# Kernel optimization log

Hardware: AMD Instinct MI355X
Metric: run time of the kernel (lower is better)

The kernel has to match this reference:

```python
import jax, jax.numpy as jnp
import numpy as np

N = 50000      # total nodes across all graphs
E = 1600000    # edges
G = 500        # graphs in batch
F = 128        # input node features
K = 5          # Chebyshev order


def setup_inputs() -> dict:
    key = jax.random.key(0)
    ks = jax.random.split(key, 12)
    x = jax.random.normal(ks[0], (N, F), dtype=jnp.float32)
    edge_index = jax.random.randint(ks[1], (2, E), 0, N)
    edge_attr = jax.random.uniform(ks[2], (E,), dtype=jnp.float32)
    batch = jnp.sort(jax.random.randint(ks[3], (N,), 0, G))
    s = 0.05
    W1 = jax.random.normal(ks[4], (K, F, 64), dtype=jnp.float32) * s
    b1 = jnp.zeros((64,), jnp.float32)
    W2 = jax.random.normal(ks[5], (K, 64, 64), dtype=jnp.float32) * s
    b2 = jnp.zeros((64,), jnp.float32)
    W3 = jax.random.normal(ks[6], (K, 64, 128), dtype=jnp.float32) * s
    b3 = jnp.zeros((128,), jnp.float32)
    Wl = jax.random.normal(ks[7], (128, 2), dtype=jnp.float32) * s
    bl = jnp.zeros((2,), jnp.float32)
    return {"x": x, "edge_index": edge_index, "edge_attr": edge_attr,
            "batch": batch, "W1": W1, "b1": b1, "W2": W2, "b2": b2,
            "W3": W3, "b3": b3, "Wl": Wl, "bl": bl}


def _cheb_conv(x, src, dst, w, Wk, b):
    """PyG ChebConv with lambda_max=2, sym norm: Lhat = -D^-1/2 A D^-1/2
    (the +I diag of L cancels the -I of the rescale, so only off-diag edges).
    Chebyshev recursion: Tx0=x, Tx1=Lhat x, Tx_k = 2 Lhat Tx_{k-1} - Tx_{k-2}."""
    n = x.shape[0]

    def prop(h):  # sparse matvec: out[i] = sum_{e: dst=i} w_e * h[src_e]
        return jax.ops.segment_sum(w[:, None] * h[src], dst, num_segments=n)

    Tx0 = x
    out = Tx0 @ Wk[0]
    Tx1 = prop(Tx0)
    out = out + Tx1 @ Wk[1]
    for k in range(2, Wk.shape[0]):
        Tx2 = 2.0 * prop(Tx1) - Tx0
        out = out + Tx2 @ Wk[k]
        Tx0, Tx1 = Tx1, Tx2
    return out + b


def reference(x, edge_index, edge_attr, batch, W1, b1, W2, b2, W3, b3, Wl, bl):
    src, dst = edge_index[0], edge_index[1]
    # sym-normalized scaled Laplacian edge weights (off-diagonal part)
    deg = jax.ops.segment_sum(edge_attr, src, num_segments=N)
    deg_safe = jnp.where(deg > 0, deg, 1.0)
    dinv = jnp.where(deg > 0, deg_safe ** -0.5, 0.0)
    w = -dinv[src] * edge_attr * dinv[dst]

    h = jax.nn.relu(_cheb_conv(x, src, dst, w, W1, b1))
    # dropout is identity at inference (training=False)
    h = jax.nn.relu(_cheb_conv(h, src, dst, w, W2, b2))
    h = jax.nn.relu(_cheb_conv(h, src, dst, w, W3, b3))

    # global_mean_pool over batch vector
    cnt = jax.ops.segment_sum(jnp.ones((N,), h.dtype), batch, num_segments=G)
    pooled = jax.ops.segment_sum(h, batch, num_segments=G) / jnp.maximum(cnt, 1.0)[:, None]

    logits = pooled @ Wl + bl
    return jax.nn.log_softmax(logits, axis=1)
```

## Files before the change

### kernel.cpp

```cpp
#include <hip/hip_runtime.h>
#include <hip/hip_bf16.h>

#define NN 50000
#define EE 1600000
#define GG 500

typedef __bf16 bf16x8 __attribute__((ext_vector_type(8)));
typedef float  f32x4  __attribute__((ext_vector_type(4)));

__device__ __forceinline__ float b2f(ushort u) {
  return __uint_as_float(((unsigned)u) << 16);
}
__device__ __forceinline__ ushort f2b(float f) {
  unsigned u = __float_as_uint(f);
  unsigned r = (u + 0x7fff + ((u >> 16) & 1)) >> 16;
  return (ushort)r;
}
__device__ __forceinline__ float lo16(uint v) { return __uint_as_float(v << 16); }
__device__ __forceinline__ float hi16(uint v) { return __uint_as_float(v & 0xffff0000u); }


__global__ void deg_hist_kernel(const int* __restrict__ src, const int* __restrict__ dst,
                                const float* __restrict__ ea, float* __restrict__ deg,
                                int* __restrict__ cnt, int* __restrict__ rank, int e) {
  int i = blockIdx.x * blockDim.x + threadIdx.x;
  if (i < e) {
    atomicAdd(&deg[src[i]], ea[i]);
    rank[i] = atomicAdd(&cnt[dst[i]], 1);
  }
}

__global__ void dinv_kernel(float* __restrict__ deg, int n) {
  int i = blockIdx.x * blockDim.x + threadIdx.x;
  if (i < n) { float d = deg[i]; deg[i] = (d > 0.f) ? (1.0f / sqrtf(d)) : 0.f; }
}

__global__ void scan1(const int* __restrict__ cnt, int* __restrict__ partial,
                      int* __restrict__ bsum, int n) {
  __shared__ int s[256];
  int t = threadIdx.x, i = blockIdx.x * 256 + t;
  int v = (i < n) ? ((cnt[i] + 7) & ~7) : 0;
  s[t] = v; __syncthreads();
  for (int off = 1; off < 256; off <<= 1) {
    int xv = (t >= off) ? s[t - off] : 0;
    __syncthreads(); s[t] += xv; __syncthreads();
  }
  if (i < n) partial[i] = s[t];
  if (t == 255) bsum[blockIdx.x] = s[255];
}

__global__ void scan2(int* __restrict__ bsum, int nb) {
  __shared__ int s[256];
  int t = threadIdx.x;
  int v = (t < nb) ? bsum[t] : 0;
  s[t] = v; __syncthreads();
  for (int off = 1; off < 256; off <<= 1) {
    int xv = (t >= off) ? s[t - off] : 0;
    __syncthreads(); s[t] += xv; __syncthreads();
  }
  if (t < nb) bsum[t] = s[t];
}

__global__ void scan3(const int* __restrict__ partial, const int* __restrict__ bsum,
                      int* __restrict__ rowptr, int n) {
  int i = blockIdx.x * 256 + threadIdx.x;
  if (i < n) {
    int off = (blockIdx.x > 0) ? bsum[blockIdx.x - 1] : 0;
    rowptr[i + 1] = partial[i] + off;
    if (i == 0) rowptr[0] = 0;
  }
}

__global__ void scatter_kernel(const int* __restrict__ src, const int* __restrict__ dst,
                               const float* __restrict__ ea, const float* __restrict__ dinv,
                               const int* __restrict__ rowptr, const int* __restrict__ rank,
                               uint2* __restrict__ edges, int e) {
  int i = blockIdx.x * blockDim.x + threadIdx.x;
  if (i < e) {
    int s = src[i], d = dst[i];
    float w = -dinv[s] * ea[i] * dinv[d];
    edges[rowptr[d] + rank[i]] = make_uint2((unsigned)s, __float_as_uint(w));
  }
}

__global__ void pad_kernel(const int* __restrict__ rowptr, const int* __restrict__ cnt,
                           uint2* __restrict__ edges, int n) {
  int i = blockIdx.x * 256 + threadIdx.x;
  if (i < n) {
    int c = cnt[i], p = (c + 7) & ~7, base = rowptr[i];
    for (int q = c; q < p; ++q) edges[base + q] = make_uint2(0u, 0u);
  }
}


__global__ void cvt_x(const float* __restrict__ x, ushort* __restrict__ xb, int n4) {
  int i = blockIdx.x * 256 + threadIdx.x;
  if (i < n4) {
    float4 v = ((const float4*)x)[i];
    ushort4 o;
    o.x = f2b(v.x); o.y = f2b(v.y); o.z = f2b(v.z); o.w = f2b(v.w);
    ((ushort4*)xb)[i] = o;
  }
}

__global__ void cvt_w(const float* __restrict__ W1, const float* __restrict__ W2,
                      const float* __restrict__ W3, ushort* __restrict__ Wt1,
                      ushort* __restrict__ Wt2, ushort* __restrict__ Wt3) {
  int i = blockIdx.x * 256 + threadIdx.x;
  if (i < 320 * 128) {
    int j = i / 128, k = i % 128;
    Wt1[i] = f2b(W1[((size_t)(j >> 6) * 128 + k) * 64 + (j & 63)]);
  } else if (i < 320 * 128 + 320 * 64) {
    int t = i - 320 * 128; int j = t / 64, k = t % 64;
    Wt2[t] = f2b(W2[((size_t)(j >> 6) * 64 + k) * 64 + (j & 63)]);
  } else if (i < 320 * 128 + 320 * 64 + 128 * 320) {
    int t = i - 320 * 128 - 320 * 64; int j = t / 320, k = t % 320;
    Wt3[t] = f2b(W3[(size_t)k * 128 + j]);
  }
}


template<int NADD, bool RELUB>
__global__ __launch_bounds__(256) void prop_kernel(
    const int* __restrict__ rowptr, const uint2* __restrict__ edges,
    const ushort* __restrict__ g, int sg,
    const ushort* __restrict__ a1, int sa1, float c1,
    const ushort* __restrict__ a2, int sa2, float c2,
    const float* __restrict__ bias,
    ushort* __restrict__ out, int so, int n, float alpha)
{
  int wv = blockIdx.x * 4 + (threadIdx.x >> 6);
  wv = __builtin_amdgcn_readfirstlane(wv);
  const int lane = threadIdx.x & 63;
  const int grp = lane >> 3;
  const int sub = lane & 7;
  if (wv >= n) return;
  const int e0 = __builtin_amdgcn_readfirstlane(rowptr[wv]);
  const int e1 = __builtin_amdgcn_readfirstlane(rowptr[wv + 1]);

  float ra[8] = {}, rb[8] = {};
  int j = e0;
  for (; j + 16 <= e1; j += 16) {
    uint2 pa = edges[j + grp];
    uint2 pb = edges[j + 8 + grp];
    uint4 va = *(const uint4*)&g[(size_t)pa.x * sg + sub * 8];
    uint4 vb = *(const uint4*)&g[(size_t)pb.x * sg + sub * 8];
    float wa = __uint_as_float(pa.y);
    float wb = __uint_as_float(pb.y);
    ra[0] += wa * lo16(va.x); ra[1] += wa * hi16(va.x);
    ra[2] += wa * lo16(va.y); ra[3] += wa * hi16(va.y);
    ra[4] += wa * lo16(va.z); ra[5] += wa * hi16(va.z);
    ra[6] += wa * lo16(va.w); ra[7] += wa * hi16(va.w);
    rb[0] += wb * lo16(vb.x); rb[1] += wb * hi16(vb.x);
    rb[2] += wb * lo16(vb.y); rb[3] += wb * hi16(vb.y);
    rb[4] += wb * lo16(vb.z); rb[5] += wb * hi16(vb.z);
    rb[6] += wb * lo16(vb.w); rb[7] += wb * hi16(vb.w);
  }
  if (j < e1) {
    uint2 p = edges[j + grp];
    uint4 v = *(const uint4*)&g[(size_t)p.x * sg + sub * 8];
    float w = __uint_as_float(p.y);
    ra[0] += w * lo16(v.x); ra[1] += w * hi16(v.x);
    ra[2] += w * lo16(v.y); ra[3] += w * hi16(v.y);
    ra[4] += w * lo16(v.z); ra[5] += w * hi16(v.z);
    ra[6] += w * lo16(v.w); ra[7] += w * hi16(v.w);
  }
  float r[8];
  #pragma unroll
  for (int e = 0; e < 8; ++e) {
    float t = ra[e] + rb[e];
    t += __shfl_xor(t, 8, 64);
    t += __shfl_xor(t, 16, 64);
    t += __shfl_xor(t, 32, 64);
    r[e] = alpha * t;
  }
  if constexpr (NADD >= 1) {
    uint4 u = *(const uint4*)&a1[(size_t)wv * sa1 + sub * 8];
    r[0] += c1 * lo16(u.x); r[1] += c1 * hi16(u.x);
    r[2] += c1 * lo16(u.y); r[3] += c1 * hi16(u.y);
    r[4] += c1 * lo16(u.z); r[5] += c1 * hi16(u.z);
    r[6] += c1 * lo16(u.w); r[7] += c1 * hi16(u.w);
  }
  if constexpr (NADD >= 2) {
    uint4 u = *(const uint4*)&a2[(size_t)wv * sa2 + sub * 8];
    r[0] += c2 * lo16(u.x); r[1] += c2 * hi16(u.x);
    r[2] += c2 * lo16(u.y); r[3] += c2 * hi16(u.y);
    r[4] += c2 * lo16(u.z); r[5] += c2 * hi16(u.z);
    r[6] += c2 * lo16(u.w); r[7] += c2 * hi16(u.w);
  }
  if constexpr (RELUB) {
    float4 b0 = *(const float4*)&bias[sub * 8];
    float4 b1 = *(const float4*)&bias[sub * 8 + 4];
    r[0] = fmaxf(r[0] + b0.x, 0.f); r[1] = fmaxf(r[1] + b0.y, 0.f);
    r[2] = fmaxf(r[2] + b0.z, 0.f); r[3] = fmaxf(r[3] + b0.w, 0.f);
    r[4] = fmaxf(r[4] + b1.x, 0.f); r[5] = fmaxf(r[5] + b1.y, 0.f);
    r[6] = fmaxf(r[6] + b1.z, 0.f); r[7] = fmaxf(r[7] + b1.w, 0.f);
  }
  if (grp == 0) {
    uint4 o;
    o.x = (uint)f2b(r[0]) | ((uint)f2b(r[1]) << 16);
    o.y = (uint)f2b(r[2]) | ((uint)f2b(r[3]) << 16);
    o.z = (uint)f2b(r[4]) | ((uint)f2b(r[5]) << 16);
    o.w = (uint)f2b(r[6]) | ((uint)f2b(r[7]) << 16);
    *(uint4*)&out[(size_t)wv * so + sub * 8] = o;
  }
}


template<int Ci, int Co, bool BR>
__global__ __launch_bounds__(256) void gemm_mfma(const ushort* __restrict__ A,
    const ushort* __restrict__ Wt, const float* __restrict__ bias,
    ushort* __restrict__ C, int n)
{
  const int lane = threadIdx.x & 63;
  const int wid  = threadIdx.x >> 6;
  const int rb = blockIdx.x * 256;
  const int cb = blockIdx.y * 64;
  const int lr = lane & 15;
  const int lk = (lane >> 4) << 3;
  f32x4 acc[4][4] = {};

  for (int kc = 0; kc < Ci; kc += 64) {
    bf16x8 bfrag[2][4];
    #pragma unroll
    for (int ks = 0; ks < 2; ++ks)
      #pragma unroll
      for (int nt = 0; nt < 4; ++nt)
        bfrag[ks][nt] = *(const bf16x8*)&Wt[(size_t)(cb + nt * 16 + lr) * Ci + kc + ks * 32 + lk];
    #pragma unroll
    for (int s = 0; s < 4; ++s) {
      const int row = rb + (wid * 4 + s) * 16 + lr;
      const ushort* ap = &A[(size_t)row * Ci + kc + lk];
      #pragma unroll
      for (int ks = 0; ks < 2; ++ks) {
        bf16x8 af = {};
        if (row < n) af = *(const bf16x8*)(ap + ks * 32);
        #pragma unroll
        for (int nt = 0; nt < 4; ++nt)
          acc[s][nt] = __builtin_amdgcn_mfma_f32_16x16x32_bf16(af, bfrag[ks][nt], acc[s][nt], 0, 0, 0);
      }
    }
  }

  #pragma unroll
  for (int s = 0; s < 4; ++s) {
    #pragma unroll
    for (int nt = 0; nt < 4; ++nt) {
      const int col = cb + nt * 16 + lr;
      #pragma unroll
      for (int r = 0; r < 4; ++r) {
        const int row = rb + (wid * 4 + s) * 16 + ((lane >> 4) << 2) + r;
        if (row < n) {
          float v = acc[s][nt][r];
          if constexpr (BR) v = fmaxf(v + bias[col], 0.f);
          C[(size_t)row * Co + col] = f2b(v);
        }
      }
    }
  }
}


__global__ __launch_bounds__(128) void pool_kernel(const ushort* __restrict__ h,
    const int* __restrict__ batch, float* __restrict__ pooled,
    float* __restrict__ gcnt, int n) {
  const int f = threadIdx.x;
  const int i0 = blockIdx.x * 64;
  const int iend = min(i0 + 64, n);
  int cur = batch[i0];
  float acc = 0.f;
  int run = 0;
  for (int i = i0; i < iend; ++i) {
    int b = batch[i];
    float v = b2f(h[(size_t)i * 128 + f]);
    if (b != cur) {
      atomicAdd(&pooled[cur * 128 + f], acc);
      if (f == 0) atomicAdd(&gcnt[cur], (float)run);
      acc = 0.f; run = 0; cur = b;
    }
    acc += v; run++;
  }
  atomicAdd(&pooled[cur * 128 + f], acc);
  if (f == 0) atomicAdd(&gcnt[cur], (float)run);
}

__global__ __launch_bounds__(128) void head_kernel(const float* __restrict__ pooled,
    const float* __restrict__ gcnt, const float* __restrict__ Wl,
    const float* __restrict__ bl, float* __restrict__ outp)
{
  int g = blockIdx.x, t = threadIdx.x;
  float denom = fmaxf(gcnt[g], 1.f);
  float p = pooled[g * 128 + t] / denom;
  __shared__ float s0[128], s1[128];
  s0[t] = p * Wl[t * 2 + 0];
  s1[t] = p * Wl[t * 2 + 1];
  __syncthreads();
  for (int off = 64; off > 0; off >>= 1) {
    if (t < off) { s0[t] += s0[t + off]; s1[t] += s1[t + off]; }
    __syncthreads();
  }
  if (t == 0) {
    float a = s0[0] + bl[0], b = s1[0] + bl[1];
    float m = fmaxf(a, b);
    float z = logf(expf(a - m) + expf(b - m)) + m;
    outp[g * 2 + 0] = a - z;
    outp[g * 2 + 1] = b - z;
  }
}


extern "C" void kernel_launch(void* const* d_in, const int* in_sizes, int n_in,
                              void* d_out, int out_size, void* d_ws, size_t ws_size,
                              hipStream_t stream) {
  const float* x   = (const float*)d_in[0];
  const int*   ei  = (const int*)d_in[1];
  const float* ea  = (const float*)d_in[2];
  const int* batch = (const int*)d_in[3];
  const float* W1  = (const float*)d_in[4];
  const float* lb1 = (const float*)d_in[5];
  const float* W2  = (const float*)d_in[6];
  const float* lb2 = (const float*)d_in[7];
  const float* W3  = (const float*)d_in[8];
  const float* lb3 = (const float*)d_in[9];
  const float* Wl  = (const float*)d_in[10];
  const float* bl  = (const float*)d_in[11];
  const int* srcv = ei;
  const int* dstv = ei + EE;

  char* w = (char*)d_ws;
  auto alloc = [&](size_t bytes) -> char* {
    char* p = w; w += (bytes + 255) & ~(size_t)255; return p;
  };
  float* deg    = (float*)alloc((size_t)NN * 4);
  int*   rowptr = (int*)alloc((size_t)(NN + 1) * 4);
  int*   cnt    = (int*)alloc((size_t)NN * 4);
  int*   bsum   = (int*)alloc(256 * 4);
  int*   rank   = (int*)alloc((size_t)EE * 4);
  uint2* edges  = (uint2*)alloc((size_t)(EE + 8 * NN) * 8);
  ushort* xb    = (ushort*)alloc((size_t)NN * 128 * 2);
  ushort* Acat  = (ushort*)alloc((size_t)NN * 320 * 2);
  ushort* Bcat  = (ushort*)alloc((size_t)NN * 320 * 2);
  ushort* h1    = (ushort*)alloc((size_t)NN * 64 * 2);
  ushort* Wt1   = (ushort*)alloc((size_t)320 * 128 * 2);
  ushort* Wt2   = (ushort*)alloc((size_t)320 * 64 * 2);
  ushort* Wt3   = (ushort*)alloc((size_t)128 * 320 * 2);
  float* pooled = (float*)alloc((size_t)(GG * 128 + GG) * 4);
  float* gcnt   = pooled + GG * 128;
  int*   partial = (int*)Acat;
  ushort* h3 = Bcat;

  hipMemsetAsync(deg, 0, (size_t)NN * 4, stream);
  hipMemsetAsync(cnt, 0, (size_t)NN * 4, stream);
  hipMemsetAsync(pooled, 0, (size_t)(GG * 128 + GG) * 4, stream);

  deg_hist_kernel<<<(EE + 255) / 256, 256, 0, stream>>>(srcv, dstv, ea, deg, cnt, rank, EE);
  dinv_kernel<<<(NN + 255) / 256, 256, 0, stream>>>(deg, NN);
  const int nb = (NN + 255) / 256;
  scan1<<<nb, 256, 0, stream>>>(cnt, partial, bsum, NN);
  scan2<<<1, 256, 0, stream>>>(bsum, nb);
  scan3<<<nb, 256, 0, stream>>>(partial, bsum, rowptr, NN);
  scatter_kernel<<<(EE + 255) / 256, 256, 0, stream>>>(srcv, dstv, ea, deg, rowptr, rank,
                                                       edges, EE);
  pad_kernel<<<nb, 256, 0, stream>>>(rowptr, cnt, edges, NN);

  cvt_x<<<(NN * 128 / 4 + 255) / 256, 256, 0, stream>>>(x, xb, NN * 128 / 4);
  cvt_w<<<(320 * 128 + 320 * 64 + 128 * 320 + 255) / 256, 256, 0, stream>>>(
      W1, W2, W3, Wt1, Wt2, Wt3);

  const int PG = (NN + 3) / 4;
  const int GX = (NN + 255) / 256;

  ushort* A0 = Acat + 0 * 64;  ushort* A1 = Acat + 1 * 64;  ushort* A2 = Acat + 2 * 64;
  ushort* A3 = Acat + 3 * 64;  ushort* A4 = Acat + 4 * 64;
  ushort* B0 = Bcat + 0 * 64;  ushort* B1 = Bcat + 1 * 64;  ushort* B2 = Bcat + 2 * 64;
  ushort* B3 = Bcat + 3 * 64;  ushort* B4 = Bcat + 4 * 64;
  const int S = 320;

  gemm_mfma<128, 320, false><<<dim3(GX, 5), 256, 0, stream>>>(xb, Wt1, nullptr, Acat, NN);
  prop_kernel<1, false><<<PG, 256, 0, stream>>>(rowptr, edges, A4, S, A3, S, 1.f,
      nullptr, 0, 0.f, nullptr, A3, S, NN, 2.f);
  prop_kernel<2, false><<<PG, 256, 0, stream>>>(rowptr, edges, A3, S, A2, S, 1.f,
      A4, S, -1.f, nullptr, A2, S, NN, 2.f);
  prop_kernel<2, false><<<PG, 256, 0, stream>>>(rowptr, edges, A2, S, A1, S, 1.f,
      A3, S, -1.f, nullptr, A1, S, NN, 2.f);
  prop_kernel<2, true><<<PG, 256, 0, stream>>>(rowptr, edges, A1, S, A0, S, 1.f,
      A2, S, -1.f, lb1, h1, 64, NN, 1.f);

  gemm_mfma<64, 320, false><<<dim3(GX, 5), 256, 0, stream>>>(h1, Wt2, nullptr, Bcat, NN);
  prop_kernel<1, false><<<PG, 256, 0, stream>>>(rowptr, edges, B4, S, B3, S, 1.f,
      nullptr, 0, 0.f, nullptr, B3, S, NN, 2.f);
  prop_kernel<2, false><<<PG, 256, 0, stream>>>(rowptr, edges, B3, S, B2, S, 1.f,
      B4, S, -1.f, nullptr, B2, S, NN, 2.f);
  prop_kernel<2, false><<<PG, 256, 0, stream>>>(rowptr, edges, B2, S, B1, S, 1.f,
      B3, S, -1.f, nullptr, B1, S, NN, 2.f);
  prop_kernel<2, true><<<PG, 256, 0, stream>>>(rowptr, edges, B1, S, B0, S, 1.f,
      B2, S, -1.f, lb2, A0, S, NN, 1.f);

  prop_kernel<0, false><<<PG, 256, 0, stream>>>(rowptr, edges, A0, S, nullptr, 0, 0.f,
      nullptr, 0, 0.f, nullptr, A1, S, NN, 1.f);
  prop_kernel<1, false><<<PG, 256, 0, stream>>>(rowptr, edges, A1, S, A0, S, -1.f,
      nullptr, 0, 0.f, nullptr, A2, S, NN, 2.f);
  prop_kernel<1, false><<<PG, 256, 0, stream>>>(rowptr, edges, A2, S, A1, S, -1.f,
      nullptr, 0, 0.f, nullptr, A3, S, NN, 2.f);
  prop_kernel<1, false><<<PG, 256, 0, stream>>>(rowptr, edges, A3, S, A2, S, -1.f,
      nullptr, 0, 0.f, nullptr, A4, S, NN, 2.f);
  gemm_mfma<320, 128, true><<<dim3(GX, 2), 256, 0, stream>>>(Acat, Wt3, lb3, h3, NN);

  pool_kernel<<<(NN + 63) / 64, 128, 0, stream>>>(h3, batch, pooled, gcnt, NN);
  head_kernel<<<GG, 128, 0, stream>>>(pooled, gcnt, Wl, bl, (float*)d_out);
}
```

Measured before the change: 667.4 us.

## Fuse preprocessing kernels and first GEMM into one multi-role launch

```diff
diff --git a/kernel.cpp b/kernel.cpp
--- a/kernel.cpp
+++ b/kernel.cpp
@@ -4,6 +4,11 @@
 #define NN 50000
 #define EE 1600000
 #define GG 500
+
+#define HB 6250
+#define GX1 196
+#define GB1 (GX1 * 5)
+#define CVB 240
 
 typedef __bf16 bf16x8 __attribute__((ext_vector_type(8)));
 typedef float  f32x4  __attribute__((ext_vector_type(4)));
@@ -20,25 +25,103 @@
 __device__ __forceinline__ float hi16(uint v) { return __uint_as_float(v & 0xffff0000u); }
 
 
-__global__ void deg_hist_kernel(const int* __restrict__ src, const int* __restrict__ dst,
-                                const float* __restrict__ ea, float* __restrict__ deg,
-                                int* __restrict__ cnt, int* __restrict__ rank, int e) {
-  int i = blockIdx.x * blockDim.x + threadIdx.x;
-  if (i < e) {
-    atomicAdd(&deg[src[i]], ea[i]);
-    rank[i] = atomicAdd(&cnt[dst[i]], 1);
-  }
-}
-
-__global__ void dinv_kernel(float* __restrict__ deg, int n) {
-  int i = blockIdx.x * blockDim.x + threadIdx.x;
-  if (i < n) { float d = deg[i]; deg[i] = (d > 0.f) ? (1.0f / sqrtf(d)) : 0.f; }
-}
-
-__global__ void scan1(const int* __restrict__ cnt, int* __restrict__ partial,
-                      int* __restrict__ bsum, int n) {
+__global__ __launch_bounds__(256) void mega1(
+    const int* __restrict__ src, const int* __restrict__ dst,
+    const float* __restrict__ ea, float* __restrict__ deg,
+    int* __restrict__ cnt, int* __restrict__ rank,
+    const float* __restrict__ x, const float* __restrict__ W1,
+    ushort* __restrict__ Acat,
+    const float* __restrict__ W2, const float* __restrict__ W3,
+    ushort* __restrict__ Wt2, ushort* __restrict__ Wt3)
+{
+  int b = blockIdx.x;
+  if (b < HB) {
+    int i = b * 256 + threadIdx.x;
+    if (i < EE) {
+      atomicAdd(&deg[src[i]], ea[i]);
+      rank[i] = atomicAdd(&cnt[dst[i]], 1);
+    }
+    return;
+  }
+  b -= HB;
+  if (b < GB1) {
+    const int bx = b % GX1, by = b / GX1;
+    const int lane = threadIdx.x & 63;
+    const int wid  = threadIdx.x >> 6;
+    const int rb = bx * 256;
+    const int cb = by * 64;
+    const int lr = lane & 15;
+    const int lk = (lane >> 4) << 3;
+    f32x4 acc[4][4] = {};
+    for (int kc = 0; kc < 128; kc += 64) {
+      bf16x8 bfrag[2][4];
+      #pragma unroll
+      for (int ks = 0; ks < 2; ++ks)
+        #pragma unroll
+        for (int nt = 0; nt < 4; ++nt) {
+          int col = cb + nt * 16 + lr;
+          int kk  = kc + ks * 32 + lk;
+          const float* wp = &W1[((size_t)(col >> 6) * 128 + kk) * 64 + (col & 63)];
+          union { bf16x8 v; ushort u[8]; } bu;
+          #pragma unroll
+          for (int t = 0; t < 8; ++t) bu.u[t] = f2b(wp[t * 64]);
+          bfrag[ks][nt] = bu.v;
+        }
+      #pragma unroll
+      for (int s = 0; s < 4; ++s) {
+        const int row = rb + (wid * 4 + s) * 16 + lr;
+        #pragma unroll
+        for (int ks = 0; ks < 2; ++ks) {
+          union { bf16x8 v; ushort u[8]; } au;
+          if (row < NN) {
+            const float* ap = &x[(size_t)row * 128 + kc + ks * 32 + lk];
+            float4 f0 = *(const float4*)ap;
+            float4 f1 = *(const float4*)(ap + 4);
+            au.u[0] = f2b(f0.x); au.u[1] = f2b(f0.y);
+            au.u[2] = f2b(f0.z); au.u[3] = f2b(f0.w);
+            au.u[4] = f2b(f1.x); au.u[5] = f2b(f1.y);
+            au.u[6] = f2b(f1.z); au.u[7] = f2b(f1.w);
+          } else {
+            au.v = bf16x8{};
+          }
+          #pragma unroll
+          for (int nt = 0; nt < 4; ++nt)
+            acc[s][nt] = __builtin_amdgcn_mfma_f32_16x16x32_bf16(au.v, bfrag[ks][nt],
+                                                                 acc[s][nt], 0, 0, 0);
+        }
+      }
+    }
+    #pragma unroll
+    for (int s = 0; s < 4; ++s)
+      #pragma unroll
+      for (int nt = 0; nt < 4; ++nt) {
+        const int col = cb + nt * 16 + lr;
+        #pragma unroll
+        for (int r = 0; r < 4; ++r) {
+          const int row = rb + (wid * 4 + s) * 16 + ((lane >> 4) << 2) + r;
+          if (row < NN) Acat[(size_t)row * 320 + col] = f2b(acc[s][nt][r]);
+        }
+      }
+    return;
+  }
+  b -= GB1;
+  int t = b * 256 + threadIdx.x;
+  if (t < 320 * 64) {
+    int j = t / 64, k = t % 64;
+    Wt2[t] = f2b(W2[((size_t)(j >> 6) * 64 + k) * 64 + (j & 63)]);
+  } else {
+    int t2 = t - 320 * 64;
+    int j = t2 / 320, k = t2 % 320;
+    Wt3[t2] = f2b(W3[(size_t)k * 128 + j]);
+  }
+}
+
+
+__global__ void scan1(const int* __restrict__ cnt, float* __restrict__ deg,
+                      int* __restrict__ partial, int* __restrict__ bsum, int n) {
   __shared__ int s[256];
   int t = threadIdx.x, i = blockIdx.x * 256 + t;
+  if (i < n) { float d = deg[i]; deg[i] = (d > 0.f) ? (1.0f / sqrtf(d)) : 0.f; }
   int v = (i < n) ? ((cnt[i] + 7) & ~7) : 0;
   s[t] = v; __syncthreads();
   for (int off = 1; off < 256; off <<= 1) {
@@ -62,12 +145,17 @@
 }
 
 __global__ void scan3(const int* __restrict__ partial, const int* __restrict__ bsum,
-                      int* __restrict__ rowptr, int n) {
+                      const int* __restrict__ cnt, int* __restrict__ rowptr,
+                      uint2* __restrict__ edges, int n) {
   int i = blockIdx.x * 256 + threadIdx.x;
   if (i < n) {
     int off = (blockIdx.x > 0) ? bsum[blockIdx.x - 1] : 0;
-    rowptr[i + 1] = partial[i] + off;
+    int end = partial[i] + off;
+    rowptr[i + 1] = end;
     if (i == 0) rowptr[0] = 0;
+    int c = cnt[i];
+    int start = end - ((c + 7) & ~7);
+    for (int q = start + c; q < end; ++q) edges[q] = make_uint2(0u, 0u);
   }
 }
 
@@ -80,42 +168,6 @@
     int s = src[i], d = dst[i];
     float w = -dinv[s] * ea[i] * dinv[d];
     edges[rowptr[d] + rank[i]] = make_uint2((unsigned)s, __float_as_uint(w));
-  }
-}
-
-__global__ void pad_kernel(const int* __restrict__ rowptr, const int* __restrict__ cnt,
-                           uint2* __restrict__ edges, int n) {
-  int i = blockIdx.x * 256 + threadIdx.x;
-  if (i < n) {
-    int c = cnt[i], p = (c + 7) & ~7, base = rowptr[i];
-    for (int q = c; q < p; ++q) edges[base + q] = make_uint2(0u, 0u);
-  }
-}
-
-
-__global__ void cvt_x(const float* __restrict__ x, ushort* __restrict__ xb, int n4) {
-  int i = blockIdx.x * 256 + threadIdx.x;
-  if (i < n4) {
-    float4 v = ((const float4*)x)[i];
-    ushort4 o;
-    o.x = f2b(v.x); o.y = f2b(v.y); o.z = f2b(v.z); o.w = f2b(v.w);
-    ((ushort4*)xb)[i] = o;
-  }
-}
-
-__global__ void cvt_w(const float* __restrict__ W1, const float* __restrict__ W2,
-                      const float* __restrict__ W3, ushort* __restrict__ Wt1,
-                      ushort* __restrict__ Wt2, ushort* __restrict__ Wt3) {
-  int i = blockIdx.x * 256 + threadIdx.x;
-  if (i < 320 * 128) {
-    int j = i / 128, k = i % 128;
-    Wt1[i] = f2b(W1[((size_t)(j >> 6) * 128 + k) * 64 + (j & 63)]);
-  } else if (i < 320 * 128 + 320 * 64) {
-    int t = i - 320 * 128; int j = t / 64, k = t % 64;
-    Wt2[t] = f2b(W2[((size_t)(j >> 6) * 64 + k) * 64 + (j & 63)]);
-  } else if (i < 320 * 128 + 320 * 64 + 128 * 320) {
-    int t = i - 320 * 128 - 320 * 64; int j = t / 320, k = t % 320;
-    Wt3[t] = f2b(W3[(size_t)k * 128 + j]);
   }
 }
 
@@ -243,7 +295,7 @@
   }
 
   #pragma unroll
-  for (int s = 0; s < 4; ++s) {
+  for (int s = 0; s < 4; ++s)
     #pragma unroll
     for (int nt = 0; nt < 4; ++nt) {
       const int col = cb + nt * 16 + lr;
@@ -257,7 +309,6 @@
         }
       }
     }
-  }
 }
 
 
@@ -332,40 +383,33 @@
     char* p = w; w += (bytes + 255) & ~(size_t)255; return p;
   };
   float* deg    = (float*)alloc((size_t)NN * 4);
+  int*   cnt    = (int*)alloc((size_t)NN * 4);
+  float* pooled = (float*)alloc((size_t)(GG * 128 + GG) * 4);
+  float* gcnt   = pooled + GG * 128;
+  char*  zero_end = w;
   int*   rowptr = (int*)alloc((size_t)(NN + 1) * 4);
-  int*   cnt    = (int*)alloc((size_t)NN * 4);
   int*   bsum   = (int*)alloc(256 * 4);
   int*   rank   = (int*)alloc((size_t)EE * 4);
   uint2* edges  = (uint2*)alloc((size_t)(EE + 8 * NN) * 8);
-  ushort* xb    = (ushort*)alloc((size_t)NN * 128 * 2);
   ushort* Acat  = (ushort*)alloc((size_t)NN * 320 * 2);
   ushort* Bcat  = (ushort*)alloc((size_t)NN * 320 * 2);
   ushort* h1    = (ushort*)alloc((size_t)NN * 64 * 2);
-  ushort* Wt1   = (ushort*)alloc((size_t)320 * 128 * 2);
   ushort* Wt2   = (ushort*)alloc((size_t)320 * 64 * 2);
   ushort* Wt3   = (ushort*)alloc((size_t)128 * 320 * 2);
-  float* pooled = (float*)alloc((size_t)(GG * 128 + GG) * 4);
-  float* gcnt   = pooled + GG * 128;
-  int*   partial = (int*)Acat;
+  int*   partial = (int*)Bcat;
   ushort* h3 = Bcat;
 
-  hipMemsetAsync(deg, 0, (size_t)NN * 4, stream);
-  hipMemsetAsync(cnt, 0, (size_t)NN * 4, stream);
-  hipMemsetAsync(pooled, 0, (size_t)(GG * 128 + GG) * 4, stream);
-
-  deg_hist_kernel<<<(EE + 255) / 256, 256, 0, stream>>>(srcv, dstv, ea, deg, cnt, rank, EE);
-  dinv_kernel<<<(NN + 255) / 256, 256, 0, stream>>>(deg, NN);
+  hipMemsetAsync(deg, 0, (size_t)(zero_end - (char*)deg), stream);
+
+  mega1<<<HB + GB1 + CVB, 256, 0, stream>>>(srcv, dstv, ea, deg, cnt, rank,
+                                            x, W1, Acat, W2, W3, Wt2, Wt3);
+
   const int nb = (NN + 255) / 256;
-  scan1<<<nb, 256, 0, stream>>>(cnt, partial, bsum, NN);
+  scan1<<<nb, 256, 0, stream>>>(cnt, deg, partial, bsum, NN);
   scan2<<<1, 256, 0, stream>>>(bsum, nb);
-  scan3<<<nb, 256, 0, stream>>>(partial, bsum, rowptr, NN);
+  scan3<<<nb, 256, 0, stream>>>(partial, bsum, cnt, rowptr, edges, NN);
   scatter_kernel<<<(EE + 255) / 256, 256, 0, stream>>>(srcv, dstv, ea, deg, rowptr, rank,
                                                        edges, EE);
-  pad_kernel<<<nb, 256, 0, stream>>>(rowptr, cnt, edges, NN);
-
-  cvt_x<<<(NN * 128 / 4 + 255) / 256, 256, 0, stream>>>(x, xb, NN * 128 / 4);
-  cvt_w<<<(320 * 128 + 320 * 64 + 128 * 320 + 255) / 256, 256, 0, stream>>>(
-      W1, W2, W3, Wt1, Wt2, Wt3);
 
   const int PG = (NN + 3) / 4;
   const int GX = (NN + 255) / 256;
@@ -376,7 +420,6 @@
   ushort* B3 = Bcat + 3 * 64;  ushort* B4 = Bcat + 4 * 64;
   const int S = 320;
 
-  gemm_mfma<128, 320, false><<<dim3(GX, 5), 256, 0, stream>>>(xb, Wt1, nullptr, Acat, NN);
   prop_kernel<1, false><<<PG, 256, 0, stream>>>(rowptr, edges, A4, S, A3, S, 1.f,
       nullptr, 0, 0.f, nullptr, A3, S, NN, 2.f);
   prop_kernel<2, false><<<PG, 256, 0, stream>>>(rowptr, edges, A3, S, A2, S, 1.f,
```

Result: faster. 639.8 us (-4.1%).
